# Kernel optimization log

Hardware: AMD Instinct MI355X
Metric: run time of the kernel (lower is better)

## Reference

```python
import jax, jax.numpy as jnp
import numpy as np

NUM_CHANNELS = 256
NUM_HEADS = 8
HEAD_DIM = NUM_CHANNELS // NUM_HEADS


def setup_inputs() -> dict:
    key = jax.random.key(0)
    k1, k2, k3, k4, k5 = jax.random.split(key, 5)
    C = NUM_CHANNELS
    s = 1.0 / np.sqrt(C)
    image = jax.random.normal(k1, (8, C, 32, 32), dtype=jnp.float32)
    # kqv_projection: Linear(C, 3C); mix_heads: Linear(C, C). Stored as [in, out].
    w_kqv = jax.random.uniform(k2, (C, 3 * C), minval=-s, maxval=s, dtype=jnp.float32)
    b_kqv = jax.random.uniform(k3, (3 * C,), minval=-s, maxval=s, dtype=jnp.float32)
    w_mix = jax.random.uniform(k4, (C, C), minval=-s, maxval=s, dtype=jnp.float32)
    b_mix = jax.random.uniform(k5, (C,), minval=-s, maxval=s, dtype=jnp.float32)
    return {"image": image, "w_kqv": w_kqv, "b_kqv": b_kqv, "w_mix": w_mix, "b_mix": b_mix}


def _masked_attention(seq, w_kqv, b_kqv, w_mix, b_mix):
    # seq: [N, T, C]
    N, T, C = seq.shape
    H, D = NUM_HEADS, HEAD_DIM
    projected = seq @ w_kqv + b_kqv            # [N, T, 3C]
    k, q, v = jnp.split(projected, 3, axis=-1)  # order: keys, queries, values
    # split heads -> [N, H, T, D]
    k = k.reshape(N, T, H, D).transpose(0, 2, 1, 3)
    q = q.reshape(N, T, H, D).transpose(0, 2, 1, 3)
    v = v.reshape(N, T, H, D).transpose(0, 2, 1, 3)
    logits = jnp.einsum('nhtd,nhsd->nhts', q, k) / jnp.sqrt(jnp.float32(D))
    causal = jnp.tril(jnp.ones((T, T), dtype=bool))
    logits = jnp.where(causal, logits, -jnp.inf)
    weights = jax.nn.softmax(logits, axis=-1)
    out = jnp.einsum('nhts,nhsd->nhtd', weights, v)  # [N, H, T, D]
    out = out.transpose(0, 2, 1, 3).reshape(N, T, C)  # combine heads
    return out @ w_mix + b_mix


def reference(image, w_kqv, b_kqv, w_mix, b_mix):
    N, C, Hh, Ww = image.shape
    seq = image.transpose(0, 2, 3, 1).reshape(N, Hh * Ww, C)
    attn = _masked_attention(seq, w_kqv, b_kqv, w_mix, b_mix)
    attn = attn.reshape(N, Hh, Ww, C).transpose(0, 3, 1, 2)
    return attn + image
```

## Files before the change

### kernel.cpp

```cpp
#include <hip/hip_runtime.h>
#include <math.h>

constexpr int NB  = 8;
constexpr int C   = 256;
constexpr int T   = 1024;
constexpr int NH  = 8;
constexpr int HD  = 32;
constexpr int C3  = 768;

constexpr float QSCALE = 0.25503489422229562f;

typedef __attribute__((ext_vector_type(8))) short bf16x8;
typedef __attribute__((ext_vector_type(4))) float f32x4;

__device__ inline short f2bf(float f) {
    unsigned u = __float_as_uint(f);
    u += 0x7FFF + ((u >> 16) & 1);
    return (short)(u >> 16);
}
__device__ inline short f2bf_trunc(float f) {
    return (short)(__float_as_uint(f) >> 16);
}

__device__ __forceinline__ void gl16(const void* g, void* l) {
    __builtin_amdgcn_global_load_lds(
        (const __attribute__((address_space(1))) unsigned int*)g,
        (__attribute__((address_space(3))) unsigned int*)l, 16, 0, 0);
}

__global__ __launch_bounds__(256) void prep_tc(const float* __restrict__ image,
                                               const float* __restrict__ wkqv,
                                               const float* __restrict__ wmix,
                                               short* __restrict__ Xb,
                                               short* __restrict__ Wkb,
                                               short* __restrict__ Wmb) {
    __shared__ float tile[64][65];
    const int bid = blockIdx.x;
    const int tid = threadIdx.x;
    const float* src; short* dst;
    int Cc, r0, c0;
    if (bid < 512) {
        const int nb = bid >> 6, t = bid & 63;
        src = image + (size_t)nb * C * T;
        dst = Xb + (size_t)nb * T * C;
        Cc = T; r0 = (t & 3) * 64; c0 = (t >> 2) * 64;
    } else if (bid < 560) {
        const int t = bid - 512;
        src = wkqv; dst = Wkb;
        Cc = C3; r0 = (t & 3) * 64; c0 = (t >> 2) * 64;
    } else {
        const int t = bid - 560;
        src = wmix; dst = Wmb;
        Cc = C; r0 = (t & 3) * 64; c0 = (t >> 2) * 64;
    }
    const int lr = tid >> 4, lc = (tid & 15) * 4;
    #pragma unroll
    for (int p = 0; p < 4; ++p) {
        float4 v = *(const float4*)&src[(size_t)(r0 + 16 * p + lr) * Cc + c0 + lc];
        tile[16 * p + lr][lc + 0] = v.x;
        tile[16 * p + lr][lc + 1] = v.y;
        tile[16 * p + lr][lc + 2] = v.z;
        tile[16 * p + lr][lc + 3] = v.w;
    }
    __syncthreads();
    const int wc = tid >> 2, wr = (tid & 3) * 16;
    bf16x8 v0, v1;
    #pragma unroll
    for (int e = 0; e < 8; ++e) v0[e] = f2bf(tile[wr + e][wc]);
    #pragma unroll
    for (int e = 0; e < 8; ++e) v1[e] = f2bf(tile[wr + 8 + e][wc]);
    short* o = dst + (size_t)(c0 + wc) * C + r0 + wr;
    *(bf16x8*)&o[0] = v0;
    *(bf16x8*)&o[8] = v1;
}

__global__ __launch_bounds__(256) void kqv_mfma(const short* __restrict__ Xb,
                                                const short* __restrict__ Wkb,
                                                const float* __restrict__ bkqv,
                                                short* __restrict__ Kb,
                                                short* __restrict__ Qb,
                                                short* __restrict__ Vtb) {
    __shared__ __align__(16) short As[128 * 64];
    __shared__ __align__(16) short Bs[64 * 64];
    const int tid = threadIdx.x;
    const int n0 = blockIdx.x * 64;
    const int m0 = blockIdx.y * 128;
    const int nb = m0 >> 10, t0 = m0 & 1023;
    const int wv = tid >> 6, lane = tid & 63;
    const int m = lane & 15, quad = lane >> 4;

    const short* Xn = Xb + (size_t)nb * T * C + (size_t)t0 * C;
    const short* Wn = Wkb + (size_t)n0 * C;

    f32x4 acc[2][4];
    const f32x4 z = {0.f, 0.f, 0.f, 0.f};
    #pragma unroll
    for (int i = 0; i < 2; ++i)
        #pragma unroll
        for (int j = 0; j < 4; ++j) acc[i][j] = z;

    const int sx = (m & 7) << 4;

    for (int k0 = 0; k0 < C; k0 += 64) {
        #pragma unroll
        for (int p = 0; p < 4; ++p) {
            const int o = p * 4096 + tid * 16;
            const int row = o >> 7;
            const int cb = (o & 127) ^ ((row & 7) << 4);
            gl16(Xn + (size_t)row * C + k0 + (cb >> 1), (char*)As + o);
        }
        #pragma unroll
        for (int p = 0; p < 2; ++p) {
            const int o = p * 4096 + tid * 16;
            const int row = o >> 7;
            const int cb = (o & 127) ^ ((row & 7) << 4);
            gl16(Wn + (size_t)row * C + k0 + (cb >> 1), (char*)Bs + o);
        }
        __syncthreads();

        bf16x8 a[2][2], b[2][4];
        #pragma unroll
        for (int kk = 0; kk < 2; ++kk) {
            #pragma unroll
            for (int i = 0; i < 2; ++i)
                a[kk][i] = *(const bf16x8*)((const char*)As +
                            (32 * wv + 16 * i + m) * 128 + ((kk * 64 + quad * 16) ^ sx));
            #pragma unroll
            for (int j = 0; j < 4; ++j)
                b[kk][j] = *(const bf16x8*)((const char*)Bs +
                            (16 * j + m) * 128 + ((kk * 64 + quad * 16) ^ sx));
        }
        #pragma unroll
        for (int kk = 0; kk < 2; ++kk)
            #pragma unroll
            for (int i = 0; i < 2; ++i)
                #pragma unroll
                for (int j = 0; j < 4; ++j)
                    acc[i][j] = __builtin_amdgcn_mfma_f32_16x16x32_bf16(a[kk][i], b[kk][j], acc[i][j], 0, 0, 0);
        __syncthreads();
    }

    #pragma unroll
    for (int j = 0; j < 4; ++j) {
        int jj = n0 + 16 * j + m;
        int chunk = jj >> 8, hh = (jj >> 5) & 7, d = jj & 31;
        float bias = bkqv[jj];
        if (chunk < 2) {
            short* dst = (chunk == 0) ? Kb : Qb;
            float mul = (chunk == 1) ? QSCALE : 1.0f;
            size_t base = (size_t)(nb * NH + hh) * T * HD + d;
            #pragma unroll
            for (int i = 0; i < 2; ++i) {
                int t = t0 + 32 * wv + 16 * i + 4 * quad;
                #pragma unroll
                for (int r = 0; r < 4; ++r)
                    dst[base + (size_t)(t + r) * HD] = f2bf((acc[i][j][r] + bias) * mul);
            }
        } else {
            size_t base = (size_t)(nb * NH + hh) * (16 * 2048) + (size_t)d * 64;
            #pragma unroll
            for (int i = 0; i < 2; ++i) {
                #pragma unroll
                for (int r = 0; r < 4; ++r) {
                    int t = t0 + 32 * wv + 16 * i + 4 * quad + r;
                    Vtb[base + (size_t)(t >> 6) * 2048 + (t & 63)] = f2bf(acc[i][j][r] + bias);
                }
            }
        }
    }
}

__global__ __launch_bounds__(256) void attn_mfma(const short* __restrict__ Kb,
                                                 const short* __restrict__ Qb,
                                                 const short* __restrict__ Vtb,
                                                 short* __restrict__ attnb) {
    const int qb = (blockIdx.z & 4) ? 7 - blockIdx.x : blockIdx.x;
    const int h  = blockIdx.y;
    const int nb = blockIdx.z;
    const int tid  = threadIdx.x;
    const int wv   = tid >> 6;
    const int lane = tid & 63;
    const int m    = lane & 15;
    const int quad = lane >> 4;

    __shared__ __align__(16) short Ps[128][72];

    const int q0  = qb * 128;
    const int nst = 2 * qb + 2;
    const size_t hb = (size_t)(nb * NH + h) * T * HD;
    const short* Kp = Kb + hb;
    const short* Qp = Qb + hb;
    const short* Vp = Vtb + (size_t)(nb * NH + h) * (16 * 2048);
    const f32x4 z = {0.f, 0.f, 0.f, 0.f};

    bf16x8 aq[2];
    #pragma unroll
    for (int i = 0; i < 2; ++i)
        aq[i] = *(const bf16x8*)&Qp[(size_t)(q0 + 32 * wv + 16 * i + m) * HD + 8 * quad];

    bf16x8 bk[4], vb[2][2];
    #pragma unroll
    for (int j = 0; j < 4; ++j)
        bk[j] = *(const bf16x8*)&Kp[(size_t)(16 * j + m) * HD + 8 * quad];
    #pragma unroll
    for (int kc = 0; kc < 2; ++kc)
        #pragma unroll
        for (int hf = 0; hf < 2; ++hf)
            vb[kc][hf] = *(const bf16x8*)&Vp[(size_t)(16 * hf + m) * 64 + 32 * kc + 8 * quad];

    f32x4 O[2][2] = {{z, z}, {z, z}};
    float lp[2][4] = {};

    auto step = [&](const int st, const bool msk) {
        f32x4 S[2][4];
        #pragma unroll
        for (int i = 0; i < 2; ++i)
            #pragma unroll
            for (int j = 0; j < 4; ++j)
                S[i][j] = __builtin_amdgcn_mfma_f32_16x16x32_bf16(aq[i], bk[j], z, 0, 0, 0);

        if (st + 1 < nst) {
            #pragma unroll
            for (int j = 0; j < 4; ++j)
                bk[j] = *(const bf16x8*)&Kp[(size_t)((st + 1) * 64 + 16 * j + m) * HD + 8 * quad];
        }

        const int s0 = st * 64;
        #pragma unroll
        for (int i = 0; i < 2; ++i) {
            const int qr_base = q0 + 32 * wv + 16 * i + 4 * quad;
            #pragma unroll
            for (int j = 0; j < 4; ++j) {
                const int sc = s0 + 16 * j + m;
                #pragma unroll
                for (int r = 0; r < 4; ++r) {
                    float e = __builtin_amdgcn_exp2f(S[i][j][r]);
                    if (msk && sc > qr_base + r) e = 0.f;
                    lp[i][r] += e;
                    Ps[32 * wv + 16 * i + 4 * quad + r][16 * j + m] = f2bf_trunc(e);
                }
            }
        }

        #pragma unroll
        for (int kc = 0; kc < 2; ++kc) {
            bf16x8 ap0 = *(const bf16x8*)&Ps[32 * wv + m][32 * kc + 8 * quad];
            bf16x8 ap1 = *(const bf16x8*)&Ps[32 * wv + 16 + m][32 * kc + 8 * quad];
            O[0][0] = __builtin_amdgcn_mfma_f32_16x16x32_bf16(ap0, vb[kc][0], O[0][0], 0, 0, 0);
            O[0][1] = __builtin_amdgcn_mfma_f32_16x16x32_bf16(ap0, vb[kc][1], O[0][1], 0, 0, 0);
            O[1][0] = __builtin_amdgcn_mfma_f32_16x16x32_bf16(ap1, vb[kc][0], O[1][0], 0, 0, 0);
            O[1][1] = __builtin_amdgcn_mfma_f32_16x16x32_bf16(ap1, vb[kc][1], O[1][1], 0, 0, 0);
        }

        if (st + 1 < nst) {
            const short* Vn = Vp + (size_t)(st + 1) * 2048;
            #pragma unroll
            for (int kc = 0; kc < 2; ++kc)
                #pragma unroll
                for (int hf = 0; hf < 2; ++hf)
                    vb[kc][hf] = *(const bf16x8*)&Vn[(size_t)(16 * hf + m) * 64 + 32 * kc + 8 * quad];
        }
    };

    const int mq = 2 * qb;
    for (int st = 0; st < mq; ++st) step(st, false);
    step(mq, true);
    step(mq + 1, true);

    #pragma unroll
    for (int i = 0; i < 2; ++i)
        #pragma unroll
        for (int r = 0; r < 4; ++r) {
            float l = lp[i][r];
            l += __shfl_xor(l, 1);
            l += __shfl_xor(l, 2);
            l += __shfl_xor(l, 4);
            l += __shfl_xor(l, 8);
            float inv = 1.f / l;
            int row = q0 + 32 * wv + 16 * i + 4 * quad + r;
            short* op = attnb + ((size_t)(nb * T + row)) * C + h * HD;
            op[m]      = f2bf(O[i][0][r] * inv);
            op[16 + m] = f2bf(O[i][1][r] * inv);
        }
}

__global__ __launch_bounds__(256) void mix_mfma(const short* __restrict__ attnb,
                                                const short* __restrict__ Wmb,
                                                const float* __restrict__ bmix,
                                                const float* __restrict__ image,
                                                float* __restrict__ out) {
    __shared__ __align__(16) short Bs[64][264];
    const int tid = threadIdx.x;
    const int n0 = blockIdx.x * 64;
    const int m0 = blockIdx.y * 64;
    const int nb = m0 >> 10, t0 = m0 & 1023;
    const int wv = tid >> 6, lane = tid & 63;
    const int m = lane & 15, quad = lane >> 4;

    {
        const short* wrow = Wmb + (size_t)(n0 + (tid >> 2)) * C + (tid & 3) * 64;
        short* brow = &Bs[tid >> 2][(tid & 3) * 64];
        #pragma unroll
        for (int g = 0; g < 8; ++g)
            *(bf16x8*)&brow[8 * g] = *(const bf16x8*)&wrow[8 * g];
    }
    __syncthreads();

    f32x4 acc[4];
    const f32x4 z = {0.f, 0.f, 0.f, 0.f};
    #pragma unroll
    for (int j = 0; j < 4; ++j) acc[j] = z;

    #pragma unroll
    for (int k0 = 0; k0 < C; k0 += 32) {
        bf16x8 a = *(const bf16x8*)&attnb[(size_t)(m0 + 16 * wv + m) * C + k0 + 8 * quad];
        bf16x8 b[4];
        #pragma unroll
        for (int j = 0; j < 4; ++j) b[j] = *(const bf16x8*)&Bs[16 * j + m][k0 + 8 * quad];
        #pragma unroll
        for (int j = 0; j < 4; ++j)
            acc[j] = __builtin_amdgcn_mfma_f32_16x16x32_bf16(a, b[j], acc[j], 0, 0, 0);
    }

    const int tb = t0 + 16 * wv + 4 * quad;
    #pragma unroll
    for (int j = 0; j < 4; ++j) {
        int c = n0 + 16 * j + m;
        float bias = bmix[c];
        size_t o = (size_t)(nb * C + c) * T + tb;
        float4 img = *(const float4*)&image[o];
        float4 res = { acc[j][0] + bias + img.x,
                       acc[j][1] + bias + img.y,
                       acc[j][2] + bias + img.z,
                       acc[j][3] + bias + img.w };
        *(float4*)&out[o] = res;
    }
}

extern "C" void kernel_launch(void* const* d_in, const int* in_sizes, int n_in,
                              void* d_out, int out_size, void* d_ws, size_t ws_size,
                              hipStream_t stream) {
    const float* image = (const float*)d_in[0];
    const float* w_kqv = (const float*)d_in[1];
    const float* b_kqv = (const float*)d_in[2];
    const float* w_mix = (const float*)d_in[3];
    const float* b_mix = (const float*)d_in[4];
    float* out = (float*)d_out;

    short* Xb    = (short*)d_ws;
    short* Wkb   = Xb  + (size_t)NB * T * C;
    short* Wmb   = Wkb + (size_t)C3 * C;
    short* Kb    = Wmb + (size_t)C * C;
    short* Qb    = Kb  + (size_t)NB * NH * T * HD;
    short* Vtb   = Qb  + (size_t)NB * NH * T * HD;
    short* attnb = Vtb + (size_t)NB * NH * T * HD;

    prep_tc<<<576, 256, 0, stream>>>(image, w_kqv, w_mix, Xb, Wkb, Wmb);
    kqv_mfma<<<dim3(C3 / 64, NB * T / 128), 256, 0, stream>>>(Xb, Wkb, b_kqv, Kb, Qb, Vtb);
    attn_mfma<<<dim3(8, NH, NB), 256, 0, stream>>>(Kb, Qb, Vtb, attnb);
    mix_mfma<<<dim3(C / 64, NB * T / 64), 256, 0, stream>>>(attnb, Wmb, b_mix, image, out);
}
```

Baseline: 105.1 us.

## Keep attention probabilities in registers via transposed QK^T and double-buffer KQV GEMM

The attention kernel computes S transposed (K as the A operand) so that each lane's softmax outputs already form the A-operand fragment of a 16x16x16 MFMA. This removes the shared-memory round trip for P, and the row-sum reduction becomes a cross-quad shuffle. Separately, the KQV projection GEMM double-buffers its LDS tiles so the next K-slice loads are issued before the current MFMAs, with one barrier per iteration instead of two. The trade-offs are twice as many smaller-K MFMAs in the PV product, narrower V loads, and double the LDS footprint in the projection kernel.

```diff
diff --git a/kernel.cpp b/kernel.cpp
--- a/kernel.cpp
+++ b/kernel.cpp
@@ -11,6 +11,7 @@
 constexpr float QSCALE = 0.25503489422229562f;
 
 typedef __attribute__((ext_vector_type(8))) short bf16x8;
+typedef __attribute__((ext_vector_type(4))) short bf16x4;
 typedef __attribute__((ext_vector_type(4))) float f32x4;
 
 __device__ inline short f2bf(float f) {
@@ -20,6 +21,10 @@
 }
 __device__ inline short f2bf_trunc(float f) {
     return (short)(__float_as_uint(f) >> 16);
+}
+
+__device__ __forceinline__ f32x4 mfma16(bf16x4 a, bf16x4 b, f32x4 c) {
+    return __builtin_amdgcn_mfma_f32_16x16x16bf16_1k(a, b, c, 0, 0, 0);
 }
 
 __device__ __forceinline__ void gl16(const void* g, void* l) {
@@ -80,8 +85,8 @@
                                                 short* __restrict__ Kb,
                                                 short* __restrict__ Qb,
                                                 short* __restrict__ Vtb) {
-    __shared__ __align__(16) short As[128 * 64];
-    __shared__ __align__(16) short Bs[64 * 64];
+    __shared__ __align__(16) short As[2][128 * 64];
+    __shared__ __align__(16) short Bs[2][64 * 64];
     const int tid = threadIdx.x;
     const int n0 = blockIdx.x * 64;
     const int m0 = blockIdx.y * 128;
@@ -101,33 +106,39 @@
 
     const int sx = (m & 7) << 4;
 
-    for (int k0 = 0; k0 < C; k0 += 64) {
+    auto stage = [&](int buf, int k0) {
         #pragma unroll
         for (int p = 0; p < 4; ++p) {
             const int o = p * 4096 + tid * 16;
             const int row = o >> 7;
             const int cb = (o & 127) ^ ((row & 7) << 4);
-            gl16(Xn + (size_t)row * C + k0 + (cb >> 1), (char*)As + o);
+            gl16(Xn + (size_t)row * C + k0 + (cb >> 1), (char*)As[buf] + o);
         }
         #pragma unroll
         for (int p = 0; p < 2; ++p) {
             const int o = p * 4096 + tid * 16;
             const int row = o >> 7;
             const int cb = (o & 127) ^ ((row & 7) << 4);
-            gl16(Wn + (size_t)row * C + k0 + (cb >> 1), (char*)Bs + o);
-        }
-        __syncthreads();
+            gl16(Wn + (size_t)row * C + k0 + (cb >> 1), (char*)Bs[buf] + o);
+        }
+    };
+
+    stage(0, 0);
+    __syncthreads();
+    int cur = 0;
+    for (int t = 0; t < 4; ++t) {
+        if (t < 3) stage(cur ^ 1, 64 * (t + 1));
 
         bf16x8 a[2][2], b[2][4];
         #pragma unroll
         for (int kk = 0; kk < 2; ++kk) {
             #pragma unroll
             for (int i = 0; i < 2; ++i)
-                a[kk][i] = *(const bf16x8*)((const char*)As +
+                a[kk][i] = *(const bf16x8*)((const char*)As[cur] +
                             (32 * wv + 16 * i + m) * 128 + ((kk * 64 + quad * 16) ^ sx));
             #pragma unroll
             for (int j = 0; j < 4; ++j)
-                b[kk][j] = *(const bf16x8*)((const char*)Bs +
+                b[kk][j] = *(const bf16x8*)((const char*)Bs[cur] +
                             (16 * j + m) * 128 + ((kk * 64 + quad * 16) ^ sx));
         }
         #pragma unroll
@@ -137,7 +148,9 @@
                 #pragma unroll
                 for (int j = 0; j < 4; ++j)
                     acc[i][j] = __builtin_amdgcn_mfma_f32_16x16x32_bf16(a[kk][i], b[kk][j], acc[i][j], 0, 0, 0);
-        __syncthreads();
+
+        if (t < 3) __syncthreads();
+        cur ^= 1;
     }
 
     #pragma unroll
@@ -183,8 +196,6 @@
     const int m    = lane & 15;
     const int quad = lane >> 4;
 
-    __shared__ __align__(16) short Ps[128][72];
-
     const int q0  = qb * 128;
     const int nst = 2 * qb + 2;
     const size_t hb = (size_t)(nb * NH + h) * T * HD;
@@ -198,18 +209,19 @@
     for (int i = 0; i < 2; ++i)
         aq[i] = *(const bf16x8*)&Qp[(size_t)(q0 + 32 * wv + 16 * i + m) * HD + 8 * quad];
 
-    bf16x8 bk[4], vb[2][2];
+    bf16x8 bk[4];
+    bf16x4 vb[4][2];
     #pragma unroll
     for (int j = 0; j < 4; ++j)
         bk[j] = *(const bf16x8*)&Kp[(size_t)(16 * j + m) * HD + 8 * quad];
     #pragma unroll
-    for (int kc = 0; kc < 2; ++kc)
+    for (int j = 0; j < 4; ++j)
         #pragma unroll
         for (int hf = 0; hf < 2; ++hf)
-            vb[kc][hf] = *(const bf16x8*)&Vp[(size_t)(16 * hf + m) * 64 + 32 * kc + 8 * quad];
+            vb[j][hf] = *(const bf16x4*)&Vp[(size_t)(16 * hf + m) * 64 + 16 * j + 4 * quad];
 
     f32x4 O[2][2] = {{z, z}, {z, z}};
-    float lp[2][4] = {};
+    float lp[2] = {0.f, 0.f};
 
     auto step = [&](const int st, const bool msk) {
         f32x4 S[2][4];
@@ -217,7 +229,7 @@
         for (int i = 0; i < 2; ++i)
             #pragma unroll
             for (int j = 0; j < 4; ++j)
-                S[i][j] = __builtin_amdgcn_mfma_f32_16x16x32_bf16(aq[i], bk[j], z, 0, 0, 0);
+                S[i][j] = __builtin_amdgcn_mfma_f32_16x16x32_bf16(bk[j], aq[i], z, 0, 0, 0);
 
         if (st + 1 < nst) {
             #pragma unroll
@@ -226,39 +238,38 @@
         }
 
         const int s0 = st * 64;
+        bf16x4 pa[2][4];
         #pragma unroll
         for (int i = 0; i < 2; ++i) {
-            const int qr_base = q0 + 32 * wv + 16 * i + 4 * quad;
+            const int qr = q0 + 32 * wv + 16 * i + m;
             #pragma unroll
             for (int j = 0; j < 4; ++j) {
-                const int sc = s0 + 16 * j + m;
+                const int kb = s0 + 16 * j + 4 * quad;
                 #pragma unroll
                 for (int r = 0; r < 4; ++r) {
                     float e = __builtin_amdgcn_exp2f(S[i][j][r]);
-                    if (msk && sc > qr_base + r) e = 0.f;
-                    lp[i][r] += e;
-                    Ps[32 * wv + 16 * i + 4 * quad + r][16 * j + m] = f2bf_trunc(e);
+                    if (msk && kb + r > qr) e = 0.f;
+                    lp[i] += e;
+                    pa[i][j][r] = f2bf_trunc(e);
                 }
             }
         }
 
         #pragma unroll
-        for (int kc = 0; kc < 2; ++kc) {
-            bf16x8 ap0 = *(const bf16x8*)&Ps[32 * wv + m][32 * kc + 8 * quad];
-            bf16x8 ap1 = *(const bf16x8*)&Ps[32 * wv + 16 + m][32 * kc + 8 * quad];
-            O[0][0] = __builtin_amdgcn_mfma_f32_16x16x32_bf16(ap0, vb[kc][0], O[0][0], 0, 0, 0);
-            O[0][1] = __builtin_amdgcn_mfma_f32_16x16x32_bf16(ap0, vb[kc][1], O[0][1], 0, 0, 0);
-            O[1][0] = __builtin_amdgcn_mfma_f32_16x16x32_bf16(ap1, vb[kc][0], O[1][0], 0, 0, 0);
-            O[1][1] = __builtin_amdgcn_mfma_f32_16x16x32_bf16(ap1, vb[kc][1], O[1][1], 0, 0, 0);
-        }
+        for (int j = 0; j < 4; ++j)
+            #pragma unroll
+            for (int i = 0; i < 2; ++i) {
+                O[i][0] = mfma16(pa[i][j], vb[j][0], O[i][0]);
+                O[i][1] = mfma16(pa[i][j], vb[j][1], O[i][1]);
+            }
 
         if (st + 1 < nst) {
             const short* Vn = Vp + (size_t)(st + 1) * 2048;
             #pragma unroll
-            for (int kc = 0; kc < 2; ++kc)
+            for (int j = 0; j < 4; ++j)
                 #pragma unroll
                 for (int hf = 0; hf < 2; ++hf)
-                    vb[kc][hf] = *(const bf16x8*)&Vn[(size_t)(16 * hf + m) * 64 + 32 * kc + 8 * quad];
+                    vb[j][hf] = *(const bf16x4*)&Vn[(size_t)(16 * hf + m) * 64 + 16 * j + 4 * quad];
         }
     };
 
@@ -268,20 +279,20 @@
     step(mq + 1, true);
 
     #pragma unroll
-    for (int i = 0; i < 2; ++i)
+    for (int i = 0; i < 2; ++i) {
+        float l = lp[i];
+        l += __shfl_xor(l, 16);
+        l += __shfl_xor(l, 32);
         #pragma unroll
         for (int r = 0; r < 4; ++r) {
-            float l = lp[i][r];
-            l += __shfl_xor(l, 1);
-            l += __shfl_xor(l, 2);
-            l += __shfl_xor(l, 4);
-            l += __shfl_xor(l, 8);
-            float inv = 1.f / l;
+            float lr = __shfl(l, 4 * quad + r);
+            float inv = 1.f / lr;
             int row = q0 + 32 * wv + 16 * i + 4 * quad + r;
             short* op = attnb + ((size_t)(nb * T + row)) * C + h * HD;
             op[m]      = f2bf(O[i][0][r] * inv);
             op[16 + m] = f2bf(O[i][1][r] * inv);
         }
+    }
 }
 
 __global__ __launch_bounds__(256) void mix_mfma(const short* __restrict__ attnb,
```

New measurement: 111.2 us. 5.8% more time.
